# Performance work log

Hardware: AMD Instinct MI355X
Metric: run time of the kernel (lower is better)

## Reference

```python
import jax, jax.numpy as jnp
import numpy as np

OUT_H, OUT_W = 128, 128


def _meshgrid(h, w):
    # normalized grid in [-1, 1], homogeneous coords: [3, h*w]
    x_t = jnp.tile(jnp.linspace(-1.0, 1.0, w)[None, :], (h, 1))
    y_t = jnp.tile(jnp.linspace(-1.0, 1.0, h)[:, None], (1, w))
    ones = jnp.ones((h * w,), dtype=jnp.float32)
    return jnp.stack([x_t.ravel(), y_t.ravel(), ones], axis=0)


def _bilinear_sample(im, x, y):
    # im: [B, H, W, C]; x, y: [B, N] pixel-space coords (transformer.py convention)
    B, H, W, C = im.shape
    # map from [-1,1] to pixel coords: x = (x + 1) * W / 2 (original transformer.py)
    x = (x + 1.0) * (W / 2.0)
    y = (y + 1.0) * (H / 2.0)

    x0 = jnp.floor(x).astype(jnp.int32)
    x1 = x0 + 1
    y0 = jnp.floor(y).astype(jnp.int32)
    y1 = y0 + 1

    x0 = jnp.clip(x0, 0, W - 1)
    x1 = jnp.clip(x1, 0, W - 1)
    y0 = jnp.clip(y0, 0, H - 1)
    y1 = jnp.clip(y1, 0, H - 1)

    bidx = jnp.arange(B, dtype=jnp.int32)[:, None]  # [B, 1] broadcasts over N
    Ia = im[bidx, y0, x0]  # [B, N, C]
    Ib = im[bidx, y1, x0]
    Ic = im[bidx, y0, x1]
    Id = im[bidx, y1, x1]

    x0f = x0.astype(jnp.float32)
    x1f = x1.astype(jnp.float32)
    y0f = y0.astype(jnp.float32)
    y1f = y1.astype(jnp.float32)

    wa = ((x1f - x) * (y1f - y))[..., None]
    wb = ((x1f - x) * (y - y0f))[..., None]
    wc = ((x - x0f) * (y1f - y))[..., None]
    wd = ((x - x0f) * (y - y0f))[..., None]

    return wa * Ia + wb * Ib + wc * Ic + wd * Id  # [B, N, C]


def setup_inputs() -> dict:
    key = jax.random.key(0)
    k1, k2 = jax.random.split(key)
    B = 2048
    image = jax.random.uniform(k1, (B, 128, 128, 3), dtype=jnp.float32)
    # near-identity homographies so sampling grids stay numerically sane
    H = jnp.eye(3, dtype=jnp.float32)[None] + 0.1 * jax.random.normal(
        k2, (B, 3, 3), dtype=jnp.float32)
    return {"image": image, "H": H}


def reference(image, H):
    # SpatialTransformer.call: take channel 0, projective warp, bilinear sample
    im = image[:, :, :, 0:1]  # [B, 128, 128, 1]
    B = im.shape[0]
    grid = _meshgrid(OUT_H, OUT_W)  # [3, N]
    T = jnp.einsum('bij,jn->bin', H, grid)  # [B, 3, N]
    z = T[:, 2]
    xs = T[:, 0] / z
    ys = T[:, 1] / z
    out = _bilinear_sample(im, xs, ys)  # [B, N, 1]
    return out.reshape(-1, OUT_H, OUT_W, 1)
```

## Files before the change

kernel.cpp:

```cpp
#include <hip/hip_runtime.h>


#define IMG_H 128
#define IMG_W 128
#define NPIX  (IMG_H * IMG_W)
#define NFLT  (NPIX * 3)
#define TPB   1024

typedef float f32x4 __attribute__((ext_vector_type(4)));

__global__ __launch_bounds__(TPB, 8) void st_warp_kernel(
    const float* __restrict__ img,
    const float* __restrict__ Hm,
    float* __restrict__ out)
{
    __shared__ float sh[NPIX];

    const int b = blockIdx.x;
    const int t = threadIdx.x;
    const float* imb = img + (size_t)b * NFLT;

    const float* Hb = Hm + b * 9;
    const float h00 = Hb[0], h01 = Hb[1], h02 = Hb[2];
    const float h10 = Hb[3], h11 = Hb[4], h12 = Hb[5];
    const float h20 = Hb[6], h21 = Hb[7], h22 = Hb[8];

    #pragma unroll
    for (int p = 0; p < 4; ++p) {
        const int c = t + p * TPB;
        const float* src = imb + c * 12;
        const f32x4 v0 = *reinterpret_cast<const f32x4*>(src);
        const f32x4 v1 = *reinterpret_cast<const f32x4*>(src + 4);
        const f32x4 v2 = *reinterpret_cast<const f32x4*>(src + 8);
        f32x4 w;
        w.x = v0.x;
        w.y = v0.w;
        w.z = v1.z;
        w.w = v2.y;
        *reinterpret_cast<f32x4*>(&sh[c * 4]) = w;
    }
    __syncthreads();

    const float step = 2.0f / 127.0f;
    float* outb = out + (size_t)b * NPIX;

    #pragma unroll 1
    for (int k = 0; k < NPIX / TPB; ++k) {
        const int n = t + k * TPB;
        const int i = n >> 7;
        const int j = n & 127;

        const float yt = -1.0f + step * (float)i;
        const float xt = -1.0f + step * (float)j;
        const float Tx = h00 * xt + h01 * yt + h02;
        const float Ty = h10 * xt + h11 * yt + h12;
        const float Tz = h20 * xt + h21 * yt + h22;
        const float x = (Tx / Tz + 1.0f) * 64.0f;
        const float y = (Ty / Tz + 1.0f) * 64.0f;

        int x0 = (int)fmaxf(fminf(floorf(x), 2.0e9f), -2.0e9f);
        int y0 = (int)fmaxf(fminf(floorf(y), 2.0e9f), -2.0e9f);
        int x1 = x0 + 1, y1 = y0 + 1;
        x0 = min(max(x0, 0), IMG_W - 1);
        x1 = min(max(x1, 0), IMG_W - 1);
        y0 = min(max(y0, 0), IMG_H - 1);
        y1 = min(max(y1, 0), IMG_H - 1);
        const int xl = min(x0, IMG_W - 2);

        const float lo0 = sh[(y0 << 7) + xl];
        const float hi0 = sh[(y0 << 7) + xl + 1];
        const float lo1 = sh[(y1 << 7) + xl];
        const float hi1 = sh[(y1 << 7) + xl + 1];
        const float Ia = (x0 > xl) ? hi0 : lo0;
        const float Ic = (x1 > xl) ? hi0 : lo0;
        const float Ib = (x0 > xl) ? hi1 : lo1;
        const float Id = (x1 > xl) ? hi1 : lo1;

        const float x0f = (float)x0, x1f = (float)x1;
        const float y0f = (float)y0, y1f = (float)y1;
        const float wa = (x1f - x) * (y1f - y);
        const float wb = (x1f - x) * (y - y0f);
        const float wc = (x - x0f) * (y1f - y);
        const float wd = (x - x0f) * (y - y0f);

        __builtin_nontemporal_store(wa * Ia + wb * Ib + wc * Ic + wd * Id,
                                    outb + n);
    }
}

extern "C" void kernel_launch(void* const* d_in, const int* in_sizes, int n_in,
                              void* d_out, int out_size, void* d_ws, size_t ws_size,
                              hipStream_t stream) {
    const float* img = (const float*)d_in[0];
    const float* Hm  = (const float*)d_in[1];
    float* out = (float*)d_out;

    const int B = in_sizes[1] / 9;
    st_warp_kernel<<<B, TPB, 0, stream>>>(img, Hm, out);
}
```

Baseline: 113.4 us.

## Store staged image channel in LDS as fp16 and halve block size

```diff
diff --git a/kernel.cpp b/kernel.cpp
--- a/kernel.cpp
+++ b/kernel.cpp
@@ -5,16 +5,17 @@
 #define IMG_W 128
 #define NPIX  (IMG_H * IMG_W)
 #define NFLT  (NPIX * 3)
-#define TPB   1024
+#define TPB   512
 
-typedef float f32x4 __attribute__((ext_vector_type(4)));
+typedef float    f32x4 __attribute__((ext_vector_type(4)));
+typedef _Float16 f16x4 __attribute__((ext_vector_type(4)));
 
 __global__ __launch_bounds__(TPB, 8) void st_warp_kernel(
     const float* __restrict__ img,
     const float* __restrict__ Hm,
     float* __restrict__ out)
 {
-    __shared__ float sh[NPIX];
+    __shared__ _Float16 shh[NPIX];
 
     const int b = blockIdx.x;
     const int t = threadIdx.x;
@@ -26,35 +27,39 @@
     const float h20 = Hb[6], h21 = Hb[7], h22 = Hb[8];
 
     #pragma unroll
-    for (int p = 0; p < 4; ++p) {
+    for (int p = 0; p < 8; ++p) {
         const int c = t + p * TPB;
         const float* src = imb + c * 12;
         const f32x4 v0 = *reinterpret_cast<const f32x4*>(src);
         const f32x4 v1 = *reinterpret_cast<const f32x4*>(src + 4);
         const f32x4 v2 = *reinterpret_cast<const f32x4*>(src + 8);
-        f32x4 w;
-        w.x = v0.x;
-        w.y = v0.w;
-        w.z = v1.z;
-        w.w = v2.y;
-        *reinterpret_cast<f32x4*>(&sh[c * 4]) = w;
+        f16x4 w;
+        w.x = (_Float16)v0.x;
+        w.y = (_Float16)v0.w;
+        w.z = (_Float16)v1.z;
+        w.w = (_Float16)v2.y;
+        *reinterpret_cast<f16x4*>(&shh[c * 4]) = w;
     }
     __syncthreads();
 
     const float step = 2.0f / 127.0f;
     float* outb = out + (size_t)b * NPIX;
 
+    const int j = t & 127;
+    const float xt = -1.0f + step * (float)j;
+    const float txc = h00 * xt;
+    const float tyc = h10 * xt;
+    const float tzc = h20 * xt;
+
     #pragma unroll 1
     for (int k = 0; k < NPIX / TPB; ++k) {
         const int n = t + k * TPB;
         const int i = n >> 7;
-        const int j = n & 127;
 
         const float yt = -1.0f + step * (float)i;
-        const float xt = -1.0f + step * (float)j;
-        const float Tx = h00 * xt + h01 * yt + h02;
-        const float Ty = h10 * xt + h11 * yt + h12;
-        const float Tz = h20 * xt + h21 * yt + h22;
+        const float Tx = txc + h01 * yt + h02;
+        const float Ty = tyc + h11 * yt + h12;
+        const float Tz = tzc + h21 * yt + h22;
         const float x = (Tx / Tz + 1.0f) * 64.0f;
         const float y = (Ty / Tz + 1.0f) * 64.0f;
 
@@ -67,10 +72,10 @@
         y1 = min(max(y1, 0), IMG_H - 1);
         const int xl = min(x0, IMG_W - 2);
 
-        const float lo0 = sh[(y0 << 7) + xl];
-        const float hi0 = sh[(y0 << 7) + xl + 1];
-        const float lo1 = sh[(y1 << 7) + xl];
-        const float hi1 = sh[(y1 << 7) + xl + 1];
+        const float lo0 = (float)shh[(y0 << 7) + xl];
+        const float hi0 = (float)shh[(y0 << 7) + xl + 1];
+        const float lo1 = (float)shh[(y1 << 7) + xl];
+        const float hi1 = (float)shh[(y1 << 7) + xl + 1];
         const float Ia = (x0 > xl) ? hi0 : lo0;
         const float Ic = (x1 > xl) ? hi0 : lo0;
         const float Ib = (x0 > xl) ? hi1 : lo1;
```

Result: slower. 138.3 us (+22.0%).

## Process several images per block with register-prefetched double-buffered LDS

Applied to the files above, without the earlier changes.

```diff
diff --git a/kernel.cpp b/kernel.cpp
--- a/kernel.cpp
+++ b/kernel.cpp
@@ -6,85 +6,118 @@
 #define NPIX  (IMG_H * IMG_W)
 #define NFLT  (NPIX * 3)
 #define TPB   1024
+#define KIMG  8
 
 typedef float f32x4 __attribute__((ext_vector_type(4)));
 
-__global__ __launch_bounds__(TPB, 8) void st_warp_kernel(
+__global__ __launch_bounds__(TPB, 4) void st_warp_kernel(
     const float* __restrict__ img,
     const float* __restrict__ Hm,
     float* __restrict__ out)
 {
-    __shared__ float sh[NPIX];
+    extern __shared__ float sh[];
+    const int t  = threadIdx.x;
+    const int b0 = blockIdx.x * KIMG;
 
-    const int b = blockIdx.x;
-    const int t = threadIdx.x;
-    const float* imb = img + (size_t)b * NFLT;
-
-    const float* Hb = Hm + b * 9;
-    const float h00 = Hb[0], h01 = Hb[1], h02 = Hb[2];
-    const float h10 = Hb[3], h11 = Hb[4], h12 = Hb[5];
-    const float h20 = Hb[6], h21 = Hb[7], h22 = Hb[8];
-
-    #pragma unroll
-    for (int p = 0; p < 4; ++p) {
-        const int c = t + p * TPB;
-        const float* src = imb + c * 12;
-        const f32x4 v0 = *reinterpret_cast<const f32x4*>(src);
-        const f32x4 v1 = *reinterpret_cast<const f32x4*>(src + 4);
-        const f32x4 v2 = *reinterpret_cast<const f32x4*>(src + 8);
-        f32x4 w;
-        w.x = v0.x;
-        w.y = v0.w;
-        w.z = v1.z;
-        w.w = v2.y;
-        *reinterpret_cast<f32x4*>(&sh[c * 4]) = w;
+    {
+        const float* imb = img + (size_t)b0 * NFLT;
+        #pragma unroll
+        for (int p = 0; p < 4; ++p) {
+            const int c = t + p * TPB;
+            const float* src = imb + c * 12;
+            const f32x4 v0 = *reinterpret_cast<const f32x4*>(src);
+            const f32x4 v1 = *reinterpret_cast<const f32x4*>(src + 4);
+            const f32x4 v2 = *reinterpret_cast<const f32x4*>(src + 8);
+            f32x4 w;
+            w.x = v0.x; w.y = v0.w; w.z = v1.z; w.w = v2.y;
+            *reinterpret_cast<f32x4*>(&sh[c * 4]) = w;
+        }
     }
     __syncthreads();
 
     const float step = 2.0f / 127.0f;
-    float* outb = out + (size_t)b * NPIX;
 
     #pragma unroll 1
-    for (int k = 0; k < NPIX / TPB; ++k) {
-        const int n = t + k * TPB;
-        const int i = n >> 7;
-        const int j = n & 127;
+    for (int k = 0; k < KIMG; ++k) {
+        const int b = b0 + k;
 
-        const float yt = -1.0f + step * (float)i;
-        const float xt = -1.0f + step * (float)j;
-        const float Tx = h00 * xt + h01 * yt + h02;
-        const float Ty = h10 * xt + h11 * yt + h12;
-        const float Tz = h20 * xt + h21 * yt + h22;
-        const float x = (Tx / Tz + 1.0f) * 64.0f;
-        const float y = (Ty / Tz + 1.0f) * 64.0f;
+        f32x4 r[12];
+        if (k + 1 < KIMG) {
+            const float* imn = img + (size_t)(b + 1) * NFLT;
+            #pragma unroll
+            for (int p = 0; p < 4; ++p) {
+                const int c = t + p * TPB;
+                const float* src = imn + c * 12;
+                r[p * 3 + 0] = *reinterpret_cast<const f32x4*>(src);
+                r[p * 3 + 1] = *reinterpret_cast<const f32x4*>(src + 4);
+                r[p * 3 + 2] = *reinterpret_cast<const f32x4*>(src + 8);
+            }
+        }
 
-        int x0 = (int)fmaxf(fminf(floorf(x), 2.0e9f), -2.0e9f);
-        int y0 = (int)fmaxf(fminf(floorf(y), 2.0e9f), -2.0e9f);
-        int x1 = x0 + 1, y1 = y0 + 1;
-        x0 = min(max(x0, 0), IMG_W - 1);
-        x1 = min(max(x1, 0), IMG_W - 1);
-        y0 = min(max(y0, 0), IMG_H - 1);
-        y1 = min(max(y1, 0), IMG_H - 1);
-        const int xl = min(x0, IMG_W - 2);
+        const float* buf = sh + (k & 1) * NPIX;
+        const float* Hb = Hm + b * 9;
+        const float h00 = Hb[0], h01 = Hb[1], h02 = Hb[2];
+        const float h10 = Hb[3], h11 = Hb[4], h12 = Hb[5];
+        const float h20 = Hb[6], h21 = Hb[7], h22 = Hb[8];
+        float* outb = out + (size_t)b * NPIX;
 
-        const float lo0 = sh[(y0 << 7) + xl];
-        const float hi0 = sh[(y0 << 7) + xl + 1];
-        const float lo1 = sh[(y1 << 7) + xl];
-        const float hi1 = sh[(y1 << 7) + xl + 1];
-        const float Ia = (x0 > xl) ? hi0 : lo0;
-        const float Ic = (x1 > xl) ? hi0 : lo0;
-        const float Ib = (x0 > xl) ? hi1 : lo1;
-        const float Id = (x1 > xl) ? hi1 : lo1;
+        #pragma unroll 1
+        for (int q = 0; q < NPIX / TPB; ++q) {
+            const int n = t + q * TPB;
+            const int i = n >> 7;
+            const int j = n & 127;
 
-        const float x0f = (float)x0, x1f = (float)x1;
-        const float y0f = (float)y0, y1f = (float)y1;
-        const float wa = (x1f - x) * (y1f - y);
-        const float wb = (x1f - x) * (y - y0f);
-        const float wc = (x - x0f) * (y1f - y);
-        const float wd = (x - x0f) * (y - y0f);
+            const float yt = -1.0f + step * (float)i;
+            const float xt = -1.0f + step * (float)j;
+            const float Tx = h00 * xt + h01 * yt + h02;
+            const float Ty = h10 * xt + h11 * yt + h12;
+            const float Tz = h20 * xt + h21 * yt + h22;
+            const float x = (Tx / Tz + 1.0f) * 64.0f;
+            const float y = (Ty / Tz + 1.0f) * 64.0f;
 
-        __builtin_nontemporal_store(wa * Ia + wb * Ib + wc * Ic + wd * Id,
-                                    outb + n);
+            int x0 = (int)fmaxf(fminf(floorf(x), 2.0e9f), -2.0e9f);
+            int y0 = (int)fmaxf(fminf(floorf(y), 2.0e9f), -2.0e9f);
+            int x1 = x0 + 1, y1 = y0 + 1;
+            x0 = min(max(x0, 0), IMG_W - 1);
+            x1 = min(max(x1, 0), IMG_W - 1);
+            y0 = min(max(y0, 0), IMG_H - 1);
+            y1 = min(max(y1, 0), IMG_H - 1);
+            const int xl = min(x0, IMG_W - 2);
+
+            const float lo0 = buf[(y0 << 7) + xl];
+            const float hi0 = buf[(y0 << 7) + xl + 1];
+            const float lo1 = buf[(y1 << 7) + xl];
+            const float hi1 = buf[(y1 << 7) + xl + 1];
+            const float Ia = (x0 > xl) ? hi0 : lo0;
+            const float Ic = (x1 > xl) ? hi0 : lo0;
+            const float Ib = (x0 > xl) ? hi1 : lo1;
+            const float Id = (x1 > xl) ? hi1 : lo1;
+
+            const float x0f = (float)x0, x1f = (float)x1;
+            const float y0f = (float)y0, y1f = (float)y1;
+            const float wa = (x1f - x) * (y1f - y);
+            const float wb = (x1f - x) * (y - y0f);
+            const float wc = (x - x0f) * (y1f - y);
+            const float wd = (x - x0f) * (y - y0f);
+
+            __builtin_nontemporal_store(wa * Ia + wb * Ib + wc * Ic + wd * Id,
+                                        outb + n);
+        }
+
+        if (k + 1 < KIMG) {
+            float* nbuf = sh + ((k + 1) & 1) * NPIX;
+            #pragma unroll
+            for (int p = 0; p < 4; ++p) {
+                const int c = t + p * TPB;
+                f32x4 w;
+                w.x = r[p * 3 + 0].x;
+                w.y = r[p * 3 + 0].w;
+                w.z = r[p * 3 + 1].z;
+                w.w = r[p * 3 + 2].y;
+                *reinterpret_cast<f32x4*>(&nbuf[c * 4]) = w;
+            }
+        }
+        __syncthreads();
     }
 }
 
@@ -96,5 +129,15 @@
     float* out = (float*)d_out;
 
     const int B = in_sizes[1] / 9;
-    st_warp_kernel<<<B, TPB, 0, stream>>>(img, Hm, out);
+    const size_t lds_bytes = 2 * NPIX * sizeof(float);
+
+    static bool attr_set = false;
+    if (!attr_set) {
+        hipFuncSetAttribute((const void*)st_warp_kernel,
+                            hipFuncAttributeMaxDynamicSharedMemorySize,
+                            (int)lds_bytes);
+        attr_set = true;
+    }
+
+    st_warp_kernel<<<B / KIMG, TPB, lds_bytes, stream>>>(img, Hm, out);
 }
```

Result: slower. 137.4 us (+21.2%).
